# Performance work log

Hardware: AMD Instinct MI355X
Metric: run time of the kernel (lower is better)

The kernel has to match this reference:

```python
import jax, jax.numpy as jnp
import numpy as np

B, N, H = 64, 512, 512
HC = H // 2  # per-direction GRU hidden


def setup_inputs() -> dict:
    key = jax.random.key(0)
    ks = jax.random.split(key, 10)
    s = 0.05
    return {
        "x": jax.random.normal(ks[0], (B, N, H), jnp.float32),
        "num_nodes": jax.random.randint(ks[1], (B,), 1, N + 1),
        "w_ih": jax.random.normal(ks[2], (2, 2, 3 * HC, H), jnp.float32) * s,
        "w_hh": jax.random.normal(ks[3], (2, 2, 3 * HC, HC), jnp.float32) * s,
        "b_ih": jax.random.normal(ks[4], (2, 2, 3 * HC), jnp.float32) * s,
        "b_hh": jax.random.normal(ks[5], (2, 2, 3 * HC), jnp.float32) * s,
        "ln_gamma": jnp.ones((H,), jnp.float32),
        "ln_beta": jnp.zeros((H,), jnp.float32),
        "w_att": jax.random.normal(ks[6], (2 * H, 1), jnp.float32) * s,
        "attention_query": jax.random.normal(ks[7], (B, H), jnp.float32),
    }


def _gru_dir(x, Wih, Whh, bih, bhh, reverse):
    # x: [B, N, in] -> [B, N, HC]; single-direction GRU via lax.scan
    xg = jnp.einsum('bni,gi->bng', x, Wih) + bih  # precompute input gates [B,N,3HC]
    xs = jnp.swapaxes(xg, 0, 1)  # [N, B, 3HC]

    def step(h, xt):
        hg = jnp.einsum('bh,gh->bg', h, Whh) + bhh
        xr, xz, xn = jnp.split(xt, 3, axis=-1)
        hr, hz, hn = jnp.split(hg, 3, axis=-1)
        r = jax.nn.sigmoid(xr + hr)
        z = jax.nn.sigmoid(xz + hz)
        n = jnp.tanh(xn + r * hn)
        h2 = (1.0 - z) * n + z * h
        return h2, h2

    h0 = jnp.zeros((x.shape[0], HC), x.dtype)
    _, ys = jax.lax.scan(step, h0, xs, reverse=reverse)
    return jnp.swapaxes(ys, 0, 1)  # [B, N, HC]


def _residual_gru(x, w_ih, w_hh, b_ih, b_hh, ln_gamma, ln_beta):
    h = x
    for layer in range(2):
        fwd = _gru_dir(h, w_ih[layer, 0], w_hh[layer, 0], b_ih[layer, 0], b_hh[layer, 0], False)
        bwd = _gru_dir(h, w_ih[layer, 1], w_hh[layer, 1], b_ih[layer, 1], b_hh[layer, 1], True)
        h = jnp.concatenate([fwd, bwd], axis=-1)  # [B, N, H]
    y = h + x  # residual
    mu = jnp.mean(y, axis=-1, keepdims=True)
    var = jnp.mean((y - mu) ** 2, axis=-1, keepdims=True)
    return (y - mu) / jnp.sqrt(var + 1e-5) * ln_gamma + ln_beta


def reference(x, num_nodes, w_ih, w_hh, b_ih, b_hh, ln_gamma, ln_beta, w_att, attention_query):
    # zero-pad past each graph's node count (mirrors the torch pad-to-batch loop)
    mask = (jnp.arange(N)[None, :] < num_nodes[:, None])[:, :, None]
    xp = jnp.where(mask, x, 0.0)
    h = _residual_gru(xp, w_ih, w_hh, b_ih, b_hh, ln_gamma, ln_beta)  # [B, N, H]
    # concat([h, query]) @ w_att == h @ w_att[:H] + q @ w_att[H:]
    scores = jnp.einsum('bnh,ho->bno', h, w_att[:H]) + jnp.einsum('bh,ho->bo', attention_query, w_att[H:])[:, None, :]
    scores = jax.nn.leaky_relu(scores, negative_slope=0.01)
    w = jax.nn.softmax(scores, axis=1)  # [B, N, 1] (unmasked, as original)
    return jnp.sum(h * w, axis=1)  # [B, H]
```

## Files before the change

### kernel.cpp

```cpp
#include <hip/hip_runtime.h>
#include <stdint.h>

typedef __attribute__((ext_vector_type(8))) short short8;
typedef __attribute__((ext_vector_type(4))) float f32x4;

#define DEV static __device__ __forceinline__

#define L2E 1.4426950408889634f

DEV unsigned short f2bf(float f){
  unsigned int u = __float_as_uint(f);
  u = (u + 0x7FFFu + ((u >> 16) & 1u)) >> 16;
  return (unsigned short)u;
}
DEV float bf2f(unsigned short u){
  return __uint_as_float(((unsigned int)u) << 16);
}
DEV float frcp(float x){ return __builtin_amdgcn_rcpf(x); }
DEV float exp2a(float x){ float r; asm("v_exp_f32 %0, %1" : "=v"(r) : "v"(x)); return r; }
DEV float bfu(unsigned int u, int c){
  return c ? __uint_as_float(u & 0xFFFF0000u) : __uint_as_float(u << 16);
}
DEV float wredsum(float v){
  #pragma unroll
  for (int m = 32; m; m >>= 1) v += __shfl_xor(v, m);
  return v;
}
DEV float wredmax(float v){
  #pragma unroll
  for (int m = 32; m; m >>= 1) v = fmaxf(v, __shfl_xor(v, m));
  return v;
}

#define BB 64
#define NN 512
#define HH 512
#define HC 256

__global__ void prep_w(const float* __restrict__ wih, const float* __restrict__ whh,
                       const float* __restrict__ bih, const float* __restrict__ bhh,
                       unsigned short* __restrict__ wihb, unsigned short* __restrict__ whhb,
                       float* __restrict__ cbias)
{
  const int NW1 = 2*2*768*512;
  const int NW2 = 2*2*768*256;
  const int NCB = 2*1536;
  for (int i = blockIdx.x*256 + threadIdx.x; i < NW1+NW2+NCB; i += gridDim.x*256){
    if (i < NW1){
      const int row = (i >> 9) % 768;
      const float sc = ((row >> 8) == 2) ? 2.f*L2E : L2E;
      wihb[i] = f2bf(wih[i] * sc);
    } else if (i < NW1+NW2){
      const int k = i - NW1;
      const int row = (k >> 8) % 768;
      const float sc = ((row >> 8) == 2) ? 2.f*L2E : L2E;
      whhb[k] = f2bf(whh[k] * sc);
    } else {
      int k = i - NW1 - NW2;
      int L = k / 1536, r = k % 1536;
      int dd = r / 768, g = r % 768;
      int idx = (L*2 + dd)*768 + g;
      const float sc = (g >= 512) ? 2.f*L2E : L2E;
      cbias[k] = (bih[idx] + (g < 512 ? bhh[idx] : 0.f)) * sc;
    }
  }
}

__global__ void prep_x(const float* __restrict__ x, const int* __restrict__ nnode,
                       unsigned short* __restrict__ xpb)
{
  const int TOT4 = (BB*NN*HH) >> 2;
  for (int i = blockIdx.x*256 + threadIdx.x; i < TOT4; i += gridDim.x*256){
    const int e = i << 2;
    const int b = e >> 18;
    const int n = (e >> 9) & 511;
    float4 v = *(const float4*)(x + e);
    if (n >= nnode[b]) { v.x = 0.f; v.y = 0.f; v.z = 0.f; v.w = 0.f; }
    ushort4 o;
    o.x = f2bf(v.x); o.y = f2bf(v.y); o.z = f2bf(v.z); o.w = f2bf(v.w);
    *(ushort4*)(xpb + e) = o;
  }
}

__global__ __launch_bounds__(256, 2) void gemm_xg(
    const unsigned short* __restrict__ A,
    const unsigned short* __restrict__ W,
    const float* __restrict__ cbias,
    unsigned short* __restrict__ C)
{
  const int tid = threadIdx.x;
  const int l = tid & 63, wv = tid >> 6;
  const int col = l & 15, lq = l >> 4;
  const int n0 = blockIdx.x * 128;
  const int m0 = blockIdx.y * 128;
  const int wm = wv >> 1, wn = wv & 1;
  __shared__ char As[16384];
  __shared__ char Ws[16384];

  f32x4 acc[4][4];
  #pragma unroll
  for (int a = 0; a < 4; a++)
    #pragma unroll
    for (int b2 = 0; b2 < 4; b2++) acc[a][b2] = (f32x4){0.f,0.f,0.f,0.f};

  short8 pa[4], pw[4];
  #pragma unroll
  for (int p = 0; p < 4; p++){
    const int qq = p*256 + tid, row = qq >> 3, sl = qq & 7;
    pa[p] = *(const short8*)(A + (m0+row)*512 + sl*8);
    pw[p] = *(const short8*)(W + (n0+row)*512 + sl*8);
  }

  for (int ko = 0; ko < 8; ++ko){
    __syncthreads();
    #pragma unroll
    for (int p = 0; p < 4; p++){
      const int qq = p*256 + tid, row = qq >> 3, sl = qq & 7;
      *(short8*)(As + row*128 + ((sl ^ (row & 7)) << 4)) = pa[p];
      *(short8*)(Ws + row*128 + ((sl ^ (row & 7)) << 4)) = pw[p];
    }
    __syncthreads();
    if (ko < 7){
      #pragma unroll
      for (int p = 0; p < 4; p++){
        const int qq = p*256 + tid, row = qq >> 3, sl = qq & 7;
        pa[p] = *(const short8*)(A + (m0+row)*512 + (ko+1)*64 + sl*8);
        pw[p] = *(const short8*)(W + (n0+row)*512 + (ko+1)*64 + sl*8);
      }
    }
    #pragma unroll
    for (int kt = 0; kt < 2; kt++){
      short8 af[4], bfr[4];
      #pragma unroll
      for (int mi = 0; mi < 4; mi++){
        const int r = wm*64 + mi*16 + col;
        af[mi] = *(const short8*)(As + r*128 + ((((kt<<2)|lq) ^ (r & 7)) << 4));
      }
      #pragma unroll
      for (int ni = 0; ni < 4; ni++){
        const int r = wn*64 + ni*16 + col;
        bfr[ni] = *(const short8*)(Ws + r*128 + ((((kt<<2)|lq) ^ (r & 7)) << 4));
      }
      #pragma unroll
      for (int mi = 0; mi < 4; mi++)
        #pragma unroll
        for (int ni = 0; ni < 4; ni++)
          acc[mi][ni] = __builtin_amdgcn_mfma_f32_16x16x32_bf16(af[mi], bfr[ni], acc[mi][ni], 0, 0, 0);
    }
  }
  #pragma unroll
  for (int ni = 0; ni < 4; ni++){
    const int n = n0 + wn*64 + ni*16 + col;
    const int dirn = (n >= 768) ? 1 : 0;
    const int g = n - dirn*768;
    const int cls = g >> 8;
    const int j = g & 255;
    const int noff = dirn*768 + (j >> 5)*96 + (j & 15)*6 + cls*2 + ((j >> 4) & 1);
    const float cb = cbias[n];
    #pragma unroll
    for (int mi = 0; mi < 4; mi++){
      const int m = m0 + wm*64 + mi*16 + lq*4;
      #pragma unroll
      for (int rg = 0; rg < 4; rg++)
        C[(m + rg)*1536 + noff] = f2bf(acc[mi][ni][rg] + cb);
    }
  }
}

#define GRU_STEP(HB_R, HB_W, PF_CUR, PF_NXT, TCUR, TNEXT) do {                  \
  { const uint3 v3 = *(const uint3*)(xg + xgo + (TNEXT)*1536);                  \
    PF_NXT[0] = v3.x; PF_NXT[1] = v3.y; PF_NXT[2] = v3.z; }                     \
  f32x4 acc[6];                                                                 \
  _Pragma("unroll")                                                             \
  for (int i = 0; i < 6; i++) acc[i] = (f32x4){0.f,0.f,0.f,0.f};                \
  _Pragma("unroll")                                                             \
  for (int kt = 0; kt < 8; kt++){                                               \
    const short8 a = *(const short8*)((HB_R) + kt*64 + lq*16);                  \
    _Pragma("unroll")                                                           \
    for (int i = 0; i < 5; i++)                                                 \
      acc[i] = __builtin_amdgcn_mfma_f32_16x16x32_bf16(a, bw[i][kt], acc[i], 0, 0, 0); \
    const short8 w5 = *(const short8*)(wlds + w*10240 + kt*1024 + l*16);        \
    acc[5] = __builtin_amdgcn_mfma_f32_16x16x32_bf16(a, w5, acc[5], 0, 0, 0);   \
  }                                                                             \
  if (lq == 0){                                                                 \
    _Pragma("unroll")                                                           \
    for (int c = 0; c < 2; c++){                                                \
      const float xr = bfu(PF_CUR[0], c);                                       \
      const float xz = bfu(PF_CUR[1], c);                                       \
      const float xn = bfu(PF_CUR[2], c);                                       \
      const float r_ = frcp(1.f + exp2a(-(xr + acc[c][0])));                    \
      const float z_ = frcp(1.f + exp2a(-(xz + acc[2+c][0])));                  \
      const float tt = xn + r_*(acc[4+c][0] + bhn[c]);                          \
      const float n_ = 1.f - 2.f*frcp(1.f + exp2a(tt));                         \
      const float h0 = hreg[c];                                                 \
      const float hn2 = n_ + z_*(h0 - n_);                                      \
      hreg[c] = hn2;                                                            \
      const unsigned short hb = f2bf(hn2);                                      \
      outb[obo + (TCUR)*512 + c*16] = hb;                                       \
      *(unsigned short*)((HB_W) + (32*w + c*16 + col)*2) = hb;                  \
    }                                                                           \
  }                                                                             \
  __syncthreads();                                                              \
} while(0)

__global__ __launch_bounds__(512, 2) void gru_rec(
    const unsigned short* __restrict__ xg,
    const unsigned short* __restrict__ whhL,
    const float* __restrict__ bhhL,
    unsigned short* __restrict__ outb)
{
  const int tid = threadIdx.x;
  const int l = tid & 63, w = tid >> 6;
  const int col = l & 15, lq = l >> 4;
  const int dir = blockIdx.x >> 6, bg = blockIdx.x & 63;

  __shared__ char hbuf0[512];
  __shared__ char hbuf1[512];
  __shared__ char wlds[8*10240];

  const unsigned short* whh_d = whhL + dir*768*256;

  short8 bw[5][8];
  #pragma unroll
  for (int i = 0; i < 6; i++){
    const int nt = (i < 2) ? (2*w + i) : (i < 4) ? (16 + 2*w + (i-2)) : (32 + 2*w + (i-4));
    const int g = nt*16 + col;
    #pragma unroll
    for (int kt = 0; kt < 8; kt++){
      short8 v = *(const short8*)(whh_d + g*256 + kt*32 + lq*8);
      if (i < 5) bw[i][kt] = v;
      else *(short8*)(wlds + w*10240 + kt*1024 + l*16) = v;
    }
  }

  float bhn[2];
  bhn[0] = bhhL[dir*768 + 512 + 32*w + col] * (2.f*L2E);
  bhn[1] = bhhL[dir*768 + 512 + 32*w + 16 + col] * (2.f*L2E);

  if (tid < 128){
    ((unsigned int*)hbuf0)[tid] = 0u;
    ((unsigned int*)hbuf1)[tid] = 0u;
  }

  float hreg[2] = {0.f, 0.f};

  const int xgo = bg*(512*1536) + dir*768 + (w*16 + col)*6;
  const int obo = bg*(512*512) + dir*256 + 32*w + col;

  unsigned int pfA[3], pfB[3];
  const int t0 = dir ? 511 : 0;
  const int dstep = dir ? -1 : 1;
  {
    const uint3 v3 = *(const uint3*)(xg + xgo + t0*1536);
    pfA[0] = v3.x; pfA[1] = v3.y; pfA[2] = v3.z;
  }

  __syncthreads();

  int tc = t0;
  #pragma unroll 1
  for (int ss = 0; ss < 256; ss++){
    const int tA = tc;
    const int tB = tA + dstep;
    const int tC = (ss == 255) ? tB : (tB + dstep);
    GRU_STEP(hbuf0, hbuf1, pfA, pfB, tA, tB);
    GRU_STEP(hbuf1, hbuf0, pfB, pfA, tB, tC);
    tc = tC;
  }
}

__global__ void ln_score(
    const unsigned short* __restrict__ h2b, const float* __restrict__ x,
    const int* __restrict__ nnode,
    const float* __restrict__ gam, const float* __restrict__ bet,
    const float* __restrict__ watt,
    float* __restrict__ hln, float* __restrict__ scores)
{
  const int bidx = blockIdx.x;
  const int b = bidx >> 9, n = bidx & 511;
  const int l = threadIdx.x;
  const int base = bidx*512;
  const int i0 = l*8;
  const bool valid = n < nnode[b];

  const short8 hv = *(const short8*)(h2b + base + i0);
  float y[8];
  #pragma unroll
  for (int p = 0; p < 2; p++){
    float4 xv = (float4){0.f,0.f,0.f,0.f};
    if (valid) xv = *(const float4*)(x + base + i0 + p*4);
    y[p*4+0] = bf2f((unsigned short)hv[p*4+0]) + xv.x;
    y[p*4+1] = bf2f((unsigned short)hv[p*4+1]) + xv.y;
    y[p*4+2] = bf2f((unsigned short)hv[p*4+2]) + xv.z;
    y[p*4+3] = bf2f((unsigned short)hv[p*4+3]) + xv.w;
  }
  float s = 0.f, sq = 0.f;
  #pragma unroll
  for (int i = 0; i < 8; i++){ s += y[i]; sq += y[i]*y[i]; }
  s = wredsum(s); sq = wredsum(sq);
  const float mu = s * (1.f/512.f);
  const float rstd = rsqrtf(sq * (1.f/512.f) - mu*mu + 1e-5f);

  float dot = 0.f;
  #pragma unroll
  for (int p = 0; p < 2; p++){
    const float4 gv = *(const float4*)(gam + i0 + p*4);
    const float4 bv = *(const float4*)(bet + i0 + p*4);
    const float4 wv = *(const float4*)(watt + i0 + p*4);
    float4 o;
    o.x = (y[p*4+0] - mu)*rstd*gv.x + bv.x;
    o.y = (y[p*4+1] - mu)*rstd*gv.y + bv.y;
    o.z = (y[p*4+2] - mu)*rstd*gv.z + bv.z;
    o.w = (y[p*4+3] - mu)*rstd*gv.w + bv.w;
    dot += o.x*wv.x + o.y*wv.y + o.z*wv.z + o.w*wv.w;
    *(float4*)(hln + base + i0 + p*4) = o;
  }
  dot = wredsum(dot);
  if (l == 0) scores[bidx] = dot;
}

__global__ void attn_pool(
    const float* __restrict__ hln, const float* __restrict__ scores,
    const float* __restrict__ watt, const float* __restrict__ q,
    float* __restrict__ out)
{
  __shared__ float sc[512];
  __shared__ float red[12];
  const int tid = threadIdx.x, l = tid & 63, w = tid >> 6;
  const int b = blockIdx.x;

  float p = q[b*512 + tid]*watt[512 + tid] + q[b*512 + 256 + tid]*watt[768 + tid];
  p = wredsum(p);
  if (l == 0) red[w] = p;
  __syncthreads();
  const float qd = red[0] + red[1] + red[2] + red[3];

  float s0 = scores[b*512 + tid] + qd;        s0 = s0 > 0.f ? s0 : 0.01f*s0;
  float s1 = scores[b*512 + 256 + tid] + qd;  s1 = s1 > 0.f ? s1 : 0.01f*s1;
  float m_ = wredmax(fmaxf(s0, s1));
  if (l == 0) red[4 + w] = m_;
  __syncthreads();
  const float mx = fmaxf(fmaxf(red[4], red[5]), fmaxf(red[6], red[7]));
  const float e0 = __expf(s0 - mx), e1 = __expf(s1 - mx);
  sc[tid] = e0; sc[tid + 256] = e1;
  float ss = wredsum(e0 + e1);
  if (l == 0) red[8 + w] = ss;
  __syncthreads();
  const float rden = 1.f / (red[8] + red[9] + red[10] + red[11]);

  const int h0 = tid*2;
  float a0 = 0.f, a1 = 0.f;
  for (int t = 0; t < 512; t++){
    const float wv = sc[t];
    const float2 v = *(const float2*)(hln + (b*512 + t)*512 + h0);
    a0 += v.x*wv; a1 += v.y*wv;
  }
  out[b*512 + h0]     = a0 * rden;
  out[b*512 + h0 + 1] = a1 * rden;
}

extern "C" void kernel_launch(void* const* d_in, const int* in_sizes, int n_in,
                              void* d_out, int out_size, void* d_ws, size_t ws_size,
                              hipStream_t stream)
{
  (void)in_sizes; (void)n_in; (void)out_size; (void)ws_size;
  const float* x    = (const float*)d_in[0];
  const int*   nn   = (const int*)d_in[1];
  const float* wih  = (const float*)d_in[2];
  const float* whh  = (const float*)d_in[3];
  const float* bih  = (const float*)d_in[4];
  const float* bhh  = (const float*)d_in[5];
  const float* lg   = (const float*)d_in[6];
  const float* lb   = (const float*)d_in[7];
  const float* watt = (const float*)d_in[8];
  const float* q    = (const float*)d_in[9];
  float* out = (float*)d_out;

  char* ws = (char*)d_ws;
  unsigned short* xg_b = (unsigned short*)(ws + 0);
  unsigned short* xp_b = (unsigned short*)(ws + 100663296);
  unsigned short* h1_b = (unsigned short*)(ws + 134217728);
  unsigned short* h2_b = (unsigned short*)(ws + 167772160);
  unsigned short* wihb = (unsigned short*)(ws + 201326592);
  unsigned short* whhb = (unsigned short*)(ws + 204472320);
  float*         cbias = (float*)(ws + 206045184);
  float*        scores = (float*)(ws + 206057472);
  float*           hln = (float*)(ws + 0);

  prep_w<<<dim3(1024), dim3(256), 0, stream>>>(wih, whh, bih, bhh, wihb, whhb, cbias);
  prep_x<<<dim3(2048), dim3(256), 0, stream>>>(x, nn, xp_b);

  gemm_xg<<<dim3(12, 256), dim3(256), 0, stream>>>(xp_b, wihb, cbias, xg_b);
  gru_rec<<<dim3(128), dim3(512), 0, stream>>>(xg_b, whhb, bhh, h1_b);

  gemm_xg<<<dim3(12, 256), dim3(256), 0, stream>>>(h1_b, wihb + 1536*512, cbias + 1536, xg_b);
  gru_rec<<<dim3(128), dim3(512), 0, stream>>>(xg_b, whhb + 2*768*256, bhh + 1536, h2_b);

  ln_score<<<dim3(64*512), dim3(64), 0, stream>>>(h2_b, x, nn, lg, lb, watt, hln, scores);
  attn_pool<<<dim3(64), dim3(256), 0, stream>>>(hln, scores, watt, q, out);
}
```

Before: 1.382 ms.

## Split GRU recurrence across 16 waves with one hidden tile per wave

The recurrent GRU kernel goes from 8 waves to 16 waves per block. Each wave now owns one 16-column hidden tile and computes three gate MFMAs per k-step instead of six. Two gate weight tiles stay in registers and the third is read from an enlarged LDS buffer. This shortens the serial per-step MFMA chain and spreads the gate math over more waves, at the cost of a heavier per-step barrier with 1024 threads and more LDS use.

```diff
diff --git a/kernel.cpp b/kernel.cpp
--- a/kernel.cpp
+++ b/kernel.cpp
@@ -167,43 +167,40 @@
   }
 }
 
+#define MFMA16(a,b,c) __builtin_amdgcn_mfma_f32_16x16x32_bf16(a, b, c, 0, 0, 0)
+
 #define GRU_STEP(HB_R, HB_W, PF_CUR, PF_NXT, TCUR, TNEXT) do {                  \
   { const uint3 v3 = *(const uint3*)(xg + xgo + (TNEXT)*1536);                  \
-    PF_NXT[0] = v3.x; PF_NXT[1] = v3.y; PF_NXT[2] = v3.z; }                     \
-  f32x4 acc[6];                                                                 \
-  _Pragma("unroll")                                                             \
-  for (int i = 0; i < 6; i++) acc[i] = (f32x4){0.f,0.f,0.f,0.f};                \
+    PF_NXT[0]=v3.x; PF_NXT[1]=v3.y; PF_NXT[2]=v3.z; }                           \
+  f32x4 acc0 = (f32x4){0.f,0.f,0.f,0.f};                                        \
+  f32x4 acc1 = (f32x4){0.f,0.f,0.f,0.f};                                        \
+  f32x4 acc2 = (f32x4){0.f,0.f,0.f,0.f};                                        \
   _Pragma("unroll")                                                             \
   for (int kt = 0; kt < 8; kt++){                                               \
     const short8 a = *(const short8*)((HB_R) + kt*64 + lq*16);                  \
-    _Pragma("unroll")                                                           \
-    for (int i = 0; i < 5; i++)                                                 \
-      acc[i] = __builtin_amdgcn_mfma_f32_16x16x32_bf16(a, bw[i][kt], acc[i], 0, 0, 0); \
-    const short8 w5 = *(const short8*)(wlds + w*10240 + kt*1024 + l*16);        \
-    acc[5] = __builtin_amdgcn_mfma_f32_16x16x32_bf16(a, w5, acc[5], 0, 0, 0);   \
+    acc0 = MFMA16(a, bw[0][kt], acc0);                                          \
+    acc1 = MFMA16(a, bw[1][kt], acc1);                                          \
+    const short8 w3 = *(const short8*)(wlds + w*8192 + kt*1024 + l*16);         \
+    acc2 = MFMA16(a, w3, acc2);                                                 \
   }                                                                             \
   if (lq == 0){                                                                 \
-    _Pragma("unroll")                                                           \
-    for (int c = 0; c < 2; c++){                                                \
-      const float xr = bfu(PF_CUR[0], c);                                       \
-      const float xz = bfu(PF_CUR[1], c);                                       \
-      const float xn = bfu(PF_CUR[2], c);                                       \
-      const float r_ = frcp(1.f + exp2a(-(xr + acc[c][0])));                    \
-      const float z_ = frcp(1.f + exp2a(-(xz + acc[2+c][0])));                  \
-      const float tt = xn + r_*(acc[4+c][0] + bhn[c]);                          \
-      const float n_ = 1.f - 2.f*frcp(1.f + exp2a(tt));                         \
-      const float h0 = hreg[c];                                                 \
-      const float hn2 = n_ + z_*(h0 - n_);                                      \
-      hreg[c] = hn2;                                                            \
-      const unsigned short hb = f2bf(hn2);                                      \
-      outb[obo + (TCUR)*512 + c*16] = hb;                                       \
-      *(unsigned short*)((HB_W) + (32*w + c*16 + col)*2) = hb;                  \
-    }                                                                           \
+    const float xr = bfu(PF_CUR[0], hi);                                        \
+    const float xz = bfu(PF_CUR[1], hi);                                        \
+    const float xn = bfu(PF_CUR[2], hi);                                        \
+    const float r_ = frcp(1.f + exp2a(-(xr + acc0[0])));                        \
+    const float z_ = frcp(1.f + exp2a(-(xz + acc1[0])));                        \
+    const float tt = xn + r_*(acc2[0] + bhn);                                   \
+    const float n_ = 1.f - 2.f*frcp(1.f + exp2a(tt));                           \
+    const float hn2 = n_ + z_*(hreg - n_);                                      \
+    hreg = hn2;                                                                 \
+    const unsigned short hb = f2bf(hn2);                                        \
+    outb[obo + (TCUR)*512] = hb;                                                \
+    *(unsigned short*)((HB_W) + j*2) = hb;                                      \
   }                                                                             \
   __syncthreads();                                                              \
 } while(0)
 
-__global__ __launch_bounds__(512, 2) void gru_rec(
+__global__ __launch_bounds__(1024, 4) void gru_rec(
     const unsigned short* __restrict__ xg,
     const unsigned short* __restrict__ whhL,
     const float* __restrict__ bhhL,
@@ -216,44 +213,41 @@
 
   __shared__ char hbuf0[512];
   __shared__ char hbuf1[512];
-  __shared__ char wlds[8*10240];
+  __shared__ char wlds[16*8192];
 
   const unsigned short* whh_d = whhL + dir*768*256;
 
-  short8 bw[5][8];
-  #pragma unroll
-  for (int i = 0; i < 6; i++){
-    const int nt = (i < 2) ? (2*w + i) : (i < 4) ? (16 + 2*w + (i-2)) : (32 + 2*w + (i-4));
+  short8 bw[2][8];
+  #pragma unroll
+  for (int i = 0; i < 3; i++){
+    const int nt = (i == 0) ? w : (i == 1) ? (16 + w) : (32 + w);
     const int g = nt*16 + col;
     #pragma unroll
     for (int kt = 0; kt < 8; kt++){
       short8 v = *(const short8*)(whh_d + g*256 + kt*32 + lq*8);
-      if (i < 5) bw[i][kt] = v;
-      else *(short8*)(wlds + w*10240 + kt*1024 + l*16) = v;
-    }
-  }
-
-  float bhn[2];
-  bhn[0] = bhhL[dir*768 + 512 + 32*w + col] * (2.f*L2E);
-  bhn[1] = bhhL[dir*768 + 512 + 32*w + 16 + col] * (2.f*L2E);
+      if (i < 2) bw[i][kt] = v;
+      else *(short8*)(wlds + w*8192 + kt*1024 + l*16) = v;
+    }
+  }
+
+  const int j = 16*w + col;
+  const float bhn = bhhL[dir*768 + 512 + j] * (2.f*L2E);
+  const int hi = w & 1;
 
   if (tid < 128){
     ((unsigned int*)hbuf0)[tid] = 0u;
     ((unsigned int*)hbuf1)[tid] = 0u;
   }
 
-  float hreg[2] = {0.f, 0.f};
-
-  const int xgo = bg*(512*1536) + dir*768 + (w*16 + col)*6;
-  const int obo = bg*(512*512) + dir*256 + 32*w + col;
+  float hreg = 0.f;
+  const int xgo = bg*(512*1536) + dir*768 + ((w >> 1)*16 + col)*6;
+  const int obo = bg*(512*512) + dir*256 + j;
 
   unsigned int pfA[3], pfB[3];
   const int t0 = dir ? 511 : 0;
   const int dstep = dir ? -1 : 1;
-  {
-    const uint3 v3 = *(const uint3*)(xg + xgo + t0*1536);
-    pfA[0] = v3.x; pfA[1] = v3.y; pfA[2] = v3.z;
-  }
+  { const uint3 v3 = *(const uint3*)(xg + xgo + t0*1536);
+    pfA[0] = v3.x; pfA[1] = v3.y; pfA[2] = v3.z; }
 
   __syncthreads();
 
@@ -391,10 +385,10 @@
   prep_x<<<dim3(2048), dim3(256), 0, stream>>>(x, nn, xp_b);
 
   gemm_xg<<<dim3(12, 256), dim3(256), 0, stream>>>(xp_b, wihb, cbias, xg_b);
-  gru_rec<<<dim3(128), dim3(512), 0, stream>>>(xg_b, whhb, bhh, h1_b);
+  gru_rec<<<dim3(128), dim3(1024), 0, stream>>>(xg_b, whhb, bhh, h1_b);
 
   gemm_xg<<<dim3(12, 256), dim3(256), 0, stream>>>(h1_b, wihb + 1536*512, cbias + 1536, xg_b);
-  gru_rec<<<dim3(128), dim3(512), 0, stream>>>(xg_b, whhb + 2*768*256, bhh + 1536, h2_b);
+  gru_rec<<<dim3(128), dim3(1024), 0, stream>>>(xg_b, whhb + 2*768*256, bhh + 1536, h2_b);
 
   ln_score<<<dim3(64*512), dim3(64), 0, stream>>>(h2_b, x, nn, lg, lb, watt, hln, scores);
   attn_pool<<<dim3(64), dim3(256), 0, stream>>>(hln, scores, watt, q, out);
```

Result: faster. 1.354 ms (-2.1%).
